# Optimization experiments

Measured on AMD Instinct MI355X. Metric: run time of the kernel, lower is better.

The kernel has to match this reference:

```python
import jax, jax.numpy as jnp
import numpy as np
import math

B, C, H, W = 32, 128, 32, 32
NUM_HEADS = 4
GROUPS = 32
EPS = 1e-5


def setup_inputs() -> dict:
    key = jax.random.key(0)
    ks = jax.random.split(key, 6)
    x = jax.random.normal(ks[0], (B, C, H, W), jnp.float32)
    norm_w = 1.0 + 0.1 * jax.random.normal(ks[1], (C,), jnp.float32)
    norm_b = 0.1 * jax.random.normal(ks[2], (C,), jnp.float32)
    qkv_w = jax.random.normal(ks[3], (3 * C, C), jnp.float32) / math.sqrt(C)
    proj_w = jax.random.normal(ks[4], (C, C), jnp.float32) / math.sqrt(C)
    proj_b = 0.01 * jax.random.normal(ks[5], (C,), jnp.float32)
    return {"x": x, "norm_w": norm_w, "norm_b": norm_b, "qkv_w": qkv_w,
            "proj_w": proj_w, "proj_b": proj_b}


def _group_norm(x, w, b):
    b_, c, h, w_ = x.shape
    xg = x.reshape(b_, GROUPS, c // GROUPS, h, w_)
    mu = xg.mean(axis=(2, 3, 4), keepdims=True)
    var = xg.var(axis=(2, 3, 4), keepdims=True)
    xn = ((xg - mu) * jax.lax.rsqrt(var + EPS)).reshape(b_, c, h, w_)
    return xn * w[None, :, None, None] + b[None, :, None, None]


def reference(x, norm_w, norm_b, qkv_w, proj_w, proj_b):
    b, c, h, w = x.shape
    nh = NUM_HEADS
    dh = c // nh
    hw = h * w
    xn = _group_norm(x, norm_w, norm_b)
    # 1x1 conv (no bias): [B,3C,H,W] flattened to [B,3C,HW]
    qkv = jnp.einsum('oc,bchw->bohw', qkv_w, xn).reshape(b, nh, 3 * dh, hw)
    # torch reshape (B*nh, 3C/nh, HW) + chunk(3, dim=1): per-head interleave
    q, k, v = qkv[:, :, :dh], qkv[:, :, dh:2 * dh], qkv[:, :, 2 * dh:]
    scale = 1.0 / math.sqrt(dh)
    # scale applied to BOTH q and k, as in the source
    attn = jnp.einsum('bhct,bhcs->bhts', q * scale, k * scale)  # [B,nh,HW,HW]
    attn = jax.nn.softmax(attn, axis=-1)
    hout = jnp.einsum('bhts,bhcs->bhct', attn, v).reshape(b, c, h, w)
    hout = jnp.einsum('oc,bchw->bohw', proj_w, hout) + proj_b[None, :, None, None]
    return hout + x
```

## Files before the change

### kernel.cpp

```cpp
#include <hip/hip_runtime.h>
#include <math.h>

#define BB 32
#define CC 128
#define HW 1024
#define NG 32
#define TPG 4096
#define QSZ ((size_t)BB * 4 * HW * 32)

typedef __attribute__((ext_vector_type(8))) short fragAB;
typedef __attribute__((ext_vector_type(4))) float fragC;
typedef __attribute__((ext_vector_type(8))) ushort ushort8v;

__device__ __forceinline__ ushort f2bf(float f) {
  union { float f; uint u; } v; v.f = f;
  uint r = v.u + 0x7FFFu + ((v.u >> 16) & 1u);
  return (ushort)(r >> 16);
}
__device__ __forceinline__ uint pack2(float lo, float hi) {
  return __builtin_amdgcn_perm(__float_as_uint(hi), __float_as_uint(lo), 0x07060302u);
}
__device__ __forceinline__ int vswz(int row, int g) {
  return row * 128 + 16 * (g ^ (row & 7));
}

__global__ __launch_bounds__(256) void gn_stats(const float* __restrict__ x,
    float2* __restrict__ stats, const float* __restrict__ qkvw,
    const float* __restrict__ projw, ushort* __restrict__ wq16,
    ushort* __restrict__ wp16) {
  if (blockIdx.x >= 1024) {
    int idx = (blockIdx.x - 1024) * 256 + threadIdx.x;
    if (idx < 49152) wq16[idx] = f2bf(qkvw[idx]);
    else             wp16[idx - 49152] = f2bf(projw[idx - 49152]);
    return;
  }
  int blk = blockIdx.x;
  int b = blk >> 5, g = blk & 31;
  const float4* xp4 = (const float4*)(x + ((size_t)(b * CC + g * 4)) * HW);
  float s = 0.f, s2 = 0.f;
  #pragma unroll
  for (int i = 0; i < 4; ++i) {
    float4 v = xp4[threadIdx.x + i * 256];
    s  += v.x + v.y + v.z + v.w;
    s2 += v.x * v.x + v.y * v.y + v.z * v.z + v.w * v.w;
  }
  #pragma unroll
  for (int off = 32; off; off >>= 1) {
    s  += __shfl_down(s, off, 64);
    s2 += __shfl_down(s2, off, 64);
  }
  __shared__ float ls[4], ls2[4];
  int lane = threadIdx.x & 63, wid = threadIdx.x >> 6;
  if (lane == 0) { ls[wid] = s; ls2[wid] = s2; }
  __syncthreads();
  if (threadIdx.x == 0) {
    float a  = ls[0] + ls[1] + ls[2] + ls[3];
    float a2 = ls2[0] + ls2[1] + ls2[2] + ls2[3];
    float mu = a * (1.f / TPG);
    float var = a2 * (1.f / TPG) - mu * mu;
    stats[blk] = make_float2(mu, rsqrtf(var + 1e-5f));
  }
}

__global__ __launch_bounds__(256) void mgemm_qkv(
    const ushort* __restrict__ W16, const float* __restrict__ xf,
    const float2* __restrict__ stats, const float* __restrict__ gw,
    const float* __restrict__ gb, ushort* __restrict__ Qb) {
  __shared__ ushort Xs[64 * 128];
  int b = blockIdx.z, t0 = blockIdx.x * 64;
  int tid = threadIdx.x;
  int lane = tid & 63, w = tid >> 6, lc = lane & 15, lg = lane >> 4;
  int wo = w >> 1, wt = w & 1;

  {
    int tq = tid & 15, co = tid >> 4;
    const float* xb = xf + (size_t)b * CC * HW + t0 + tq * 4;
    float wsc[8], bsc[8];
    {
      float2 s0 = stats[b * 32 + co * 2];
      float2 s1 = stats[b * 32 + co * 2 + 1];
      #pragma unroll
      for (int cc = 0; cc < 8; ++cc) {
        float rst = (cc < 4) ? s0.y : s1.y;
        float mu  = (cc < 4) ? s0.x : s1.x;
        float g = gw[co * 8 + cc];
        wsc[cc] = g * rst;
        bsc[cc] = gb[co * 8 + cc] - mu * wsc[cc];
      }
    }
    union { float4 v; float f[4]; } vv[8];
    #pragma unroll
    for (int cc = 0; cc < 8; ++cc)
      vv[cc].v = *(const float4*)&xb[(size_t)(co * 8 + cc) * HW];
    #pragma unroll
    for (int tt = 0; tt < 4; ++tt) {
      int row = tq * 4 + tt;
      ushort8v r;
      #pragma unroll
      for (int cc = 0; cc < 8; ++cc)
        r[cc] = f2bf(vv[cc].f[tt] * wsc[cc] + bsc[cc]);
      int byt = (row * 256 + co * 16) ^ ((row & 7) << 4);
      *(ushort8v*)((char*)Xs + byt) = r;
    }
  }
  __syncthreads();

  auto load_af = [&](fragAB af[2][4], int o0) {
    #pragma unroll
    for (int i = 0; i < 2; ++i)
      #pragma unroll
      for (int kc = 0; kc < 4; ++kc)
        af[i][kc] = *(const fragAB*)&W16[(size_t)(o0 + wo * 32 + i * 16 + lc) * 128 + kc * 32 + lg * 8];
  };
  auto kloop = [&](fragAB af[2][4], fragC acc[2][2]) {
    #pragma unroll
    for (int i = 0; i < 2; ++i)
      #pragma unroll
      for (int j = 0; j < 2; ++j)
        acc[i][j] = (fragC){0.f, 0.f, 0.f, 0.f};
    #pragma unroll
    for (int kc = 0; kc < 4; ++kc) {
      fragAB bf[2];
      #pragma unroll
      for (int j = 0; j < 2; ++j) {
        int row = wt * 32 + j * 16 + lc;
        int byt = (row * 256 + kc * 64 + lg * 16) ^ ((row & 7) << 4);
        bf[j] = *(const fragAB*)((const char*)Xs + byt);
      }
      #pragma unroll
      for (int i = 0; i < 2; ++i)
        #pragma unroll
        for (int j = 0; j < 2; ++j)
          acc[i][j] = __builtin_amdgcn_mfma_f32_16x16x32_bf16(af[i][kc], bf[j], acc[i][j], 0, 0, 0);
    }
  };
  auto epi = [&](fragC acc[2][2], int o0) {
    #pragma unroll
    for (int i = 0; i < 2; ++i) {
      int ob = o0 + wo * 32 + i * 16;
      int blk = ob >> 5;
      int hh = blk / 3, kind = blk % 3;
      size_t bh = (size_t)b * 4 + hh;
      float sc = (kind == 0) ? (0.03125f * 1.44269504f) : 1.f;
      #pragma unroll
      for (int j = 0; j < 2; ++j) {
        if (kind < 2) {
          ushort* dst = (kind == 0) ? Qb : (Qb + QSZ);
          int s16 = (t0 >> 4) + wt * 2 + j;
          int eo = s16 * 512 + (((ob & 16) >> 3) + (lg >> 1)) * 128 + lc * 8 + (lg & 1) * 4;
          ushort4 rv;
          rv.x = f2bf(acc[i][j][0] * sc); rv.y = f2bf(acc[i][j][1] * sc);
          rv.z = f2bf(acc[i][j][2] * sc); rv.w = f2bf(acc[i][j][3] * sc);
          *(ushort4*)&dst[bh * 32768 + eo] = rv;
        } else {
          ushort* Vb = Qb + 2 * QSZ;
          int eo = (t0 >> 6) * 2048 + ((ob & 16) >> 4) * 1024
                 + (wt * 4 + j * 2 + (lc >> 3)) * 128 + (lc & 7);
          #pragma unroll
          for (int r = 0; r < 4; ++r)
            Vb[bh * 32768 + eo + (lg * 4 + r) * 8] = f2bf(acc[i][j][r]);
        }
      }
    }
  };

  fragAB afA[2][4], afB[2][4];
  fragC acc[2][2];
  load_af(afA, 0);
  load_af(afB, 64);
  kloop(afA, acc); epi(acc, 0);   load_af(afA, 128);
  kloop(afB, acc); epi(acc, 64);  load_af(afB, 192);
  kloop(afA, acc); epi(acc, 128); load_af(afA, 256);
  kloop(afB, acc); epi(acc, 192); load_af(afB, 320);
  kloop(afA, acc); epi(acc, 256);
  kloop(afB, acc); epi(acc, 320);
}

__global__ __launch_bounds__(512) void attn9(
    const ushort* __restrict__ Qb, const ushort* __restrict__ Kb,
    const ushort* __restrict__ Vb, const ushort* __restrict__ wp16,
    const float* __restrict__ bias, const float* __restrict__ resid,
    float* __restrict__ out) {
  __shared__ char arena[33792];

  int tid = threadIdx.x;
  int w = tid >> 6, lane = tid & 63, lc = lane & 15, lg = lane >> 4;
  int lb = blockIdx.x;
  int gp = (lb & 7) * 64 + (lb >> 3);
  int b = gp >> 4, qp = gp & 15;
  int h = w >> 1, qs = w & 1;
  int bh = b * 4 + h;
  int t0 = qp * 64;
  int qt = qp * 2 + qs;

  const ushort* Qg = Qb + (size_t)bh * 32768 + (size_t)qt * 1024 + lane * 8;
  const ushort* Kg = Kb + (size_t)bh * 32768 + lane * 8;
  const ushort* Vg = Vb + (size_t)bh * 32768 + lane * 8;

  fragAB q0 = *(const fragAB*)&Qg[0];
  fragAB q1 = *(const fragAB*)&Qg[512];

  fragC a00 = {0.f,0.f,0.f,0.f}, a01 = {0.f,0.f,0.f,0.f};
  fragC a10 = {0.f,0.f,0.f,0.f}, a11 = {0.f,0.f,0.f,0.f};
  float l0 = 0.f, l1 = 0.f;
  char* PsB = arena + w * 2048;

  for (int i = 0; i < 16; ++i) {
    const ushort* Kt = Kg + i * 2048;
    const ushort* Vt = Vg + i * 2048;
    fragAB kf[4], vf[4];
    #pragma unroll
    for (int j = 0; j < 4; ++j) kf[j] = *(const fragAB*)&Kt[j * 512];
    #pragma unroll
    for (int u = 0; u < 4; ++u) vf[u] = *(const fragAB*)&Vt[u * 512];

    #pragma unroll
    for (int ts = 0; ts < 2; ++ts) {
      fragAB qf = ts ? q1 : q0;
      fragC S[4];
      #pragma unroll
      for (int j = 0; j < 4; ++j) {
        fragC z = {0.f,0.f,0.f,0.f};
        S[j] = __builtin_amdgcn_mfma_f32_16x16x32_bf16(kf[j], qf, z, 0, 0, 0);
      }
      float rs = 0.f;
      #pragma unroll
      for (int j = 0; j < 4; ++j) {
        float p0 = __builtin_amdgcn_exp2f(S[j][0]), p1 = __builtin_amdgcn_exp2f(S[j][1]);
        float p2 = __builtin_amdgcn_exp2f(S[j][2]), p3 = __builtin_amdgcn_exp2f(S[j][3]);
        rs += (p0 + p1) + (p2 + p3);
        uint2 wv2;
        wv2.x = pack2(p0, p1);
        wv2.y = pack2(p2, p3);
        int g = j * 2 + (lg >> 1);
        *(uint2*)(PsB + lc * 128 + 16 * (g ^ (lc & 7)) + (lg & 1) * 8) = wv2;
      }
      if (ts) l1 += rs; else l0 += rs;
      fragC* aA = ts ? &a01 : &a00;
      fragC* aB = ts ? &a11 : &a10;
      fragAB bp0 = *(const fragAB*)(PsB + vswz(lc, lg));
      fragAB bp1 = *(const fragAB*)(PsB + vswz(lc, 4 + lg));
      *aA = __builtin_amdgcn_mfma_f32_16x16x32_bf16(vf[0], bp0, *aA, 0, 0, 0);
      *aA = __builtin_amdgcn_mfma_f32_16x16x32_bf16(vf[1], bp1, *aA, 0, 0, 0);
      *aB = __builtin_amdgcn_mfma_f32_16x16x32_bf16(vf[2], bp0, *aB, 0, 0, 0);
      *aB = __builtin_amdgcn_mfma_f32_16x16x32_bf16(vf[3], bp1, *aB, 0, 0, 0);
    }
  }

  l0 += __shfl_xor(l0, 16); l0 += __shfl_xor(l0, 32);
  l1 += __shfl_xor(l1, 16); l1 += __shfl_xor(l1, 32);
  float il0 = 1.f / l0, il1 = 1.f / l1;

  ushort* Olds = (ushort*)(arena + 16384);
  {
    int rb = qs * 32, cb = h * 32;
    uint2 u;
    u.x = pack2(a00[0] * il0, a00[1] * il0); u.y = pack2(a00[2] * il0, a00[3] * il0);
    *(uint2*)&Olds[(rb + lc) * 136 + cb + lg * 4] = u;
    u.x = pack2(a10[0] * il0, a10[1] * il0); u.y = pack2(a10[2] * il0, a10[3] * il0);
    *(uint2*)&Olds[(rb + lc) * 136 + cb + 16 + lg * 4] = u;
    u.x = pack2(a01[0] * il1, a01[1] * il1); u.y = pack2(a01[2] * il1, a01[3] * il1);
    *(uint2*)&Olds[(rb + lc + 16) * 136 + cb + lg * 4] = u;
    u.x = pack2(a11[0] * il1, a11[1] * il1); u.y = pack2(a11[2] * il1, a11[3] * il1);
    *(uint2*)&Olds[(rb + lc + 16) * 136 + cb + 16 + lg * 4] = u;
  }
  __syncthreads();

  fragC pacc[4] = {{0.f,0.f,0.f,0.f}, {0.f,0.f,0.f,0.f},
                   {0.f,0.f,0.f,0.f}, {0.f,0.f,0.f,0.f}};
  #pragma unroll
  for (int kc = 0; kc < 4; ++kc) {
    fragAB af = *(const fragAB*)&wp16[(size_t)(16 * w + lc) * 128 + kc * 32 + lg * 8];
    #pragma unroll
    for (int j = 0; j < 4; ++j) {
      fragAB bf = *(const fragAB*)&Olds[(j * 16 + lc) * 136 + kc * 32 + lg * 8];
      pacc[j] = __builtin_amdgcn_mfma_f32_16x16x32_bf16(af, bf, pacc[j], 0, 0, 0);
    }
  }
  #pragma unroll
  for (int j = 0; j < 4; ++j) {
    int t = t0 + j * 16 + lc;
    #pragma unroll
    for (int r = 0; r < 4; ++r) {
      int o = 16 * w + lg * 4 + r;
      size_t idx = ((size_t)b * CC + o) * HW + t;
      out[idx] = pacc[j][r] + bias[o] + resid[idx];
    }
  }
}

extern "C" void kernel_launch(void* const* d_in, const int* in_sizes, int n_in,
                              void* d_out, int out_size, void* d_ws, size_t ws_size,
                              hipStream_t stream) {
  (void)in_sizes; (void)n_in; (void)out_size; (void)ws_size;
  const float* x     = (const float*)d_in[0];
  const float* gw    = (const float*)d_in[1];
  const float* gb    = (const float*)d_in[2];
  const float* qkvw  = (const float*)d_in[3];
  const float* projw = (const float*)d_in[4];
  const float* projb = (const float*)d_in[5];
  float* out = (float*)d_out;

  char* wsb = (char*)d_ws;
  ushort* Qb   = (ushort*)(wsb + ((size_t)8 << 20));
  ushort* Kb   = Qb + QSZ;
  ushort* Vb   = Qb + 2 * QSZ;
  ushort* wq16 = (ushort*)(wsb + ((size_t)32 << 20));
  ushort* wp16 = (ushort*)(wsb + ((size_t)32 << 20) + (128 << 10));
  float2* stats = (float2*)(wsb + ((size_t)32 << 20) + (256 << 10));

  gn_stats<<<dim3(BB * NG + 256), 256, 0, stream>>>(x, stats, qkvw, projw, wq16, wp16);
  mgemm_qkv<<<dim3(16, 1, BB), 256, 0, stream>>>(wq16, x, stats, gw, gb, Qb);
  attn9<<<dim3(512), 512, 0, stream>>>(Qb, Kb, Vb, wp16, projb, x, out);
}
```

Measured before the change: 58.49 us.

## Enlarge attention blocks to 128 query positions with 16 waves and 2x2 projection tiles

The fused attention+projection kernel now uses 1024-thread blocks covering 128 query positions per batch, with 16 waves (4 heads x 4 query slices). There are half as many blocks. The output projection is retiled so each wave computes a 32x32 tile and reuses A and B fragments. The O staging buffer now reuses the start of the LDS arena, which needs an extra barrier. The aim is better reuse of projection weights and fewer blocks, at the cost of a larger block that may reduce occupancy or load balance across 256 CUs.

```diff
diff --git a/kernel.cpp b/kernel.cpp
--- a/kernel.cpp
+++ b/kernel.cpp
@@ -176,22 +176,21 @@
   kloop(afB, acc); epi(acc, 320);
 }
 
-__global__ __launch_bounds__(512) void attn9(
+__global__ __launch_bounds__(1024) void attn11(
     const ushort* __restrict__ Qb, const ushort* __restrict__ Kb,
     const ushort* __restrict__ Vb, const ushort* __restrict__ wp16,
     const float* __restrict__ bias, const float* __restrict__ resid,
     float* __restrict__ out) {
-  __shared__ char arena[33792];
+  __shared__ char arena[34816];
 
   int tid = threadIdx.x;
   int w = tid >> 6, lane = tid & 63, lc = lane & 15, lg = lane >> 4;
   int lb = blockIdx.x;
-  int gp = (lb & 7) * 64 + (lb >> 3);
-  int b = gp >> 4, qp = gp & 15;
-  int h = w >> 1, qs = w & 1;
+  int gp = (lb & 7) * 32 + (lb >> 3);
+  int b = gp >> 3, qp = gp & 7;
+  int h = w & 3, qs = w >> 2;
   int bh = b * 4 + h;
-  int t0 = qp * 64;
-  int qt = qp * 2 + qs;
+  int qt = qp * 4 + qs;
 
   const ushort* Qg = Qb + (size_t)bh * 32768 + (size_t)qt * 1024 + lane * 8;
   const ushort* Kg = Kb + (size_t)bh * 32768 + lane * 8;
@@ -251,7 +250,9 @@
   l1 += __shfl_xor(l1, 16); l1 += __shfl_xor(l1, 32);
   float il0 = 1.f / l0, il1 = 1.f / l1;
 
-  ushort* Olds = (ushort*)(arena + 16384);
+  __syncthreads();
+
+  ushort* Olds = (ushort*)arena;
   {
     int rb = qs * 32, cb = h * 32;
     uint2 u;
@@ -266,27 +267,36 @@
   }
   __syncthreads();
 
-  fragC pacc[4] = {{0.f,0.f,0.f,0.f}, {0.f,0.f,0.f,0.f},
-                   {0.f,0.f,0.f,0.f}, {0.f,0.f,0.f,0.f}};
+  int oi = w & 3, tj = w >> 2;
+  fragC pacc[2][2] = {{{0.f,0.f,0.f,0.f}, {0.f,0.f,0.f,0.f}},
+                      {{0.f,0.f,0.f,0.f}, {0.f,0.f,0.f,0.f}}};
   #pragma unroll
   for (int kc = 0; kc < 4; ++kc) {
-    fragAB af = *(const fragAB*)&wp16[(size_t)(16 * w + lc) * 128 + kc * 32 + lg * 8];
-    #pragma unroll
-    for (int j = 0; j < 4; ++j) {
-      fragAB bf = *(const fragAB*)&Olds[(j * 16 + lc) * 136 + kc * 32 + lg * 8];
-      pacc[j] = __builtin_amdgcn_mfma_f32_16x16x32_bf16(af, bf, pacc[j], 0, 0, 0);
-    }
+    fragAB af[2], bf[2];
+    #pragma unroll
+    for (int i = 0; i < 2; ++i)
+      af[i] = *(const fragAB*)&wp16[(size_t)(oi * 32 + i * 16 + lc) * 128 + kc * 32 + lg * 8];
+    #pragma unroll
+    for (int j = 0; j < 2; ++j)
+      bf[j] = *(const fragAB*)&Olds[(tj * 32 + j * 16 + lc) * 136 + kc * 32 + lg * 8];
+    #pragma unroll
+    for (int i = 0; i < 2; ++i)
+      #pragma unroll
+      for (int j = 0; j < 2; ++j)
+        pacc[i][j] = __builtin_amdgcn_mfma_f32_16x16x32_bf16(af[i], bf[j], pacc[i][j], 0, 0, 0);
   }
   #pragma unroll
-  for (int j = 0; j < 4; ++j) {
-    int t = t0 + j * 16 + lc;
-    #pragma unroll
-    for (int r = 0; r < 4; ++r) {
-      int o = 16 * w + lg * 4 + r;
-      size_t idx = ((size_t)b * CC + o) * HW + t;
-      out[idx] = pacc[j][r] + bias[o] + resid[idx];
-    }
-  }
+  for (int i = 0; i < 2; ++i)
+    #pragma unroll
+    for (int j = 0; j < 2; ++j) {
+      int t = qp * 128 + tj * 32 + j * 16 + lc;
+      #pragma unroll
+      for (int r = 0; r < 4; ++r) {
+        int o = oi * 32 + i * 16 + lg * 4 + r;
+        size_t idx = ((size_t)b * CC + o) * HW + t;
+        out[idx] = pacc[i][j][r] + bias[o] + resid[idx];
+      }
+    }
 }
 
 extern "C" void kernel_launch(void* const* d_in, const int* in_sizes, int n_in,
@@ -311,5 +321,5 @@
 
   gn_stats<<<dim3(BB * NG + 256), 256, 0, stream>>>(x, stats, qkvw, projw, wq16, wp16);
   mgemm_qkv<<<dim3(16, 1, BB), 256, 0, stream>>>(wq16, x, stats, gw, gb, Qb);
-  attn9<<<dim3(512), 512, 0, stream>>>(Qb, Kb, Vb, wp16, projb, x, out);
-}
+  attn11<<<dim3(256), 1024, 0, stream>>>(Qb, Kb, Vb, wp16, projb, x, out);
+}
```

New measurement: 60.88 us. 4.1% more time.

## Switch attention to 32x32x16 MFMA with permlane-swap P transpose, no LDS

Applied to the files above, without the earlier changes.

Rewrites the attention inner loop to use 32x32x16 bf16 MFMA for both QK^T and PV. The softmax probabilities are converted into the B operand in registers using v_permlane32_swap instead of a round trip through LDS, which removes LDS writes and reads from each tile. The QKV GEMM epilogue is changed to write Q/K/V in a new layout that matches the 32x32 fragment ordering, and the LDS arena is shrunk. The larger 16-float accumulator fragments raise register pressure, and permlane32_swap is specific to newer CDNA parts.

```diff
diff --git a/kernel.cpp b/kernel.cpp
--- a/kernel.cpp
+++ b/kernel.cpp
@@ -10,6 +10,7 @@
 
 typedef __attribute__((ext_vector_type(8))) short fragAB;
 typedef __attribute__((ext_vector_type(4))) float fragC;
+typedef __attribute__((ext_vector_type(16))) float fragC16;
 typedef __attribute__((ext_vector_type(8))) ushort ushort8v;
 
 __device__ __forceinline__ ushort f2bf(float f) {
@@ -19,9 +20,6 @@
 }
 __device__ __forceinline__ uint pack2(float lo, float hi) {
   return __builtin_amdgcn_perm(__float_as_uint(hi), __float_as_uint(lo), 0x07060302u);
-}
-__device__ __forceinline__ int vswz(int row, int g) {
-  return row * 128 + 16 * (g ^ (row & 7));
 }
 
 __global__ __launch_bounds__(256) void gn_stats(const float* __restrict__ x,
@@ -142,23 +140,27 @@
       int hh = blk / 3, kind = blk % 3;
       size_t bh = (size_t)b * 4 + hh;
       float sc = (kind == 0) ? (0.03125f * 1.44269504f) : 1.f;
+      int cb = ob & 16;
       #pragma unroll
       for (int j = 0; j < 2; ++j) {
+        int t = t0 + wt * 32 + j * 16 + lc;
         if (kind < 2) {
           ushort* dst = (kind == 0) ? Qb : (Qb + QSZ);
-          int s16 = (t0 >> 4) + wt * 2 + j;
-          int eo = s16 * 512 + (((ob & 16) >> 3) + (lg >> 1)) * 128 + lc * 8 + (lg & 1) * 4;
+          int c4 = cb + lg * 4;
+          int eo = (t >> 5) * 1024 + (c4 >> 4) * 512 + (((c4 >> 3) & 1)) * 256
+                 + (t & 31) * 8 + (c4 & 7);
           ushort4 rv;
           rv.x = f2bf(acc[i][j][0] * sc); rv.y = f2bf(acc[i][j][1] * sc);
           rv.z = f2bf(acc[i][j][2] * sc); rv.w = f2bf(acc[i][j][3] * sc);
           *(ushort4*)&dst[bh * 32768 + eo] = rv;
         } else {
           ushort* Vb = Qb + 2 * QSZ;
-          int eo = (t0 >> 6) * 2048 + ((ob & 16) >> 4) * 1024
-                 + (wt * 4 + j * 2 + (lc >> 3)) * 128 + (lc & 7);
+          int sb = (t >> 4) * 512 + ((t >> 3) & 1) * 256 + (t & 7);
           #pragma unroll
-          for (int r = 0; r < 4; ++r)
-            Vb[bh * 32768 + eo + (lg * 4 + r) * 8] = f2bf(acc[i][j][r]);
+          for (int r = 0; r < 4; ++r) {
+            int c = cb + lg * 4 + r;
+            Vb[bh * 32768 + sb + c * 8] = f2bf(acc[i][j][r]);
+          }
         }
       }
     }
@@ -176,15 +178,16 @@
   kloop(afB, acc); epi(acc, 320);
 }
 
-__global__ __launch_bounds__(512) void attn9(
+__global__ __launch_bounds__(512) void attn12(
     const ushort* __restrict__ Qb, const ushort* __restrict__ Kb,
     const ushort* __restrict__ Vb, const ushort* __restrict__ wp16,
     const float* __restrict__ bias, const float* __restrict__ resid,
     float* __restrict__ out) {
-  __shared__ char arena[33792];
+  __shared__ char arena[17408];
 
   int tid = threadIdx.x;
   int w = tid >> 6, lane = tid & 63, lc = lane & 15, lg = lane >> 4;
+  int t = lane & 31, hi = lane >> 5;
   int lb = blockIdx.x;
   int gp = (lb & 7) * 64 + (lb >> 3);
   int b = gp >> 4, qp = gp & 15;
@@ -197,72 +200,71 @@
   const ushort* Kg = Kb + (size_t)bh * 32768 + lane * 8;
   const ushort* Vg = Vb + (size_t)bh * 32768 + lane * 8;
 
-  fragAB q0 = *(const fragAB*)&Qg[0];
-  fragAB q1 = *(const fragAB*)&Qg[512];
-
-  fragC a00 = {0.f,0.f,0.f,0.f}, a01 = {0.f,0.f,0.f,0.f};
-  fragC a10 = {0.f,0.f,0.f,0.f}, a11 = {0.f,0.f,0.f,0.f};
-  float l0 = 0.f, l1 = 0.f;
-  char* PsB = arena + w * 2048;
+  fragAB qf0 = *(const fragAB*)&Qg[0];
+  fragAB qf1 = *(const fragAB*)&Qg[512];
+
+  fragC16 acc = {0.f,0.f,0.f,0.f,0.f,0.f,0.f,0.f,0.f,0.f,0.f,0.f,0.f,0.f,0.f,0.f};
+  float l = 0.f;
+
+  auto stile = [&](fragAB ka, fragAB kb, fragAB va, fragAB vb) {
+    fragC16 S = {0.f,0.f,0.f,0.f,0.f,0.f,0.f,0.f,0.f,0.f,0.f,0.f,0.f,0.f,0.f,0.f};
+    S = __builtin_amdgcn_mfma_f32_32x32x16_bf16(ka, qf0, S, 0, 0, 0);
+    S = __builtin_amdgcn_mfma_f32_32x32x16_bf16(kb, qf1, S, 0, 0, 0);
+    float p[16];
+    float rs = 0.f;
+    #pragma unroll
+    for (int r = 0; r < 16; ++r) { p[r] = __builtin_amdgcn_exp2f(S[r]); rs += p[r]; }
+    l += rs;
+    uint U[8];
+    #pragma unroll
+    for (int k = 0; k < 8; ++k) U[k] = pack2(p[2 * k], p[2 * k + 1]);
+    uint A[8], Bv[8];
+    #pragma unroll
+    for (int m = 0; m < 8; ++m) {
+      uint a = U[m], bb = U[m];
+      asm volatile("v_permlane32_swap_b32 %0, %1" : "+v"(a), "+v"(bb));
+      A[m] = a; Bv[m] = bb;
+    }
+    union { uint u[4]; fragAB f; } bf;
+    bf.u[0] = hi ? A[2] : A[0];
+    bf.u[1] = hi ? A[3] : A[1];
+    bf.u[2] = hi ? Bv[2] : Bv[0];
+    bf.u[3] = hi ? Bv[3] : Bv[1];
+    acc = __builtin_amdgcn_mfma_f32_32x32x16_bf16(va, bf.f, acc, 0, 0, 0);
+    bf.u[0] = hi ? A[6] : A[4];
+    bf.u[1] = hi ? A[7] : A[5];
+    bf.u[2] = hi ? Bv[6] : Bv[4];
+    bf.u[3] = hi ? Bv[7] : Bv[5];
+    acc = __builtin_amdgcn_mfma_f32_32x32x16_bf16(vb, bf.f, acc, 0, 0, 0);
+  };
 
   for (int i = 0; i < 16; ++i) {
     const ushort* Kt = Kg + i * 2048;
     const ushort* Vt = Vg + i * 2048;
-    fragAB kf[4], vf[4];
-    #pragma unroll
-    for (int j = 0; j < 4; ++j) kf[j] = *(const fragAB*)&Kt[j * 512];
-    #pragma unroll
-    for (int u = 0; u < 4; ++u) vf[u] = *(const fragAB*)&Vt[u * 512];
-
-    #pragma unroll
-    for (int ts = 0; ts < 2; ++ts) {
-      fragAB qf = ts ? q1 : q0;
-      fragC S[4];
-      #pragma unroll
-      for (int j = 0; j < 4; ++j) {
-        fragC z = {0.f,0.f,0.f,0.f};
-        S[j] = __builtin_amdgcn_mfma_f32_16x16x32_bf16(kf[j], qf, z, 0, 0, 0);
-      }
-      float rs = 0.f;
-      #pragma unroll
-      for (int j = 0; j < 4; ++j) {
-        float p0 = __builtin_amdgcn_exp2f(S[j][0]), p1 = __builtin_amdgcn_exp2f(S[j][1]);
-        float p2 = __builtin_amdgcn_exp2f(S[j][2]), p3 = __builtin_amdgcn_exp2f(S[j][3]);
-        rs += (p0 + p1) + (p2 + p3);
-        uint2 wv2;
-        wv2.x = pack2(p0, p1);
-        wv2.y = pack2(p2, p3);
-        int g = j * 2 + (lg >> 1);
-        *(uint2*)(PsB + lc * 128 + 16 * (g ^ (lc & 7)) + (lg & 1) * 8) = wv2;
-      }
-      if (ts) l1 += rs; else l0 += rs;
-      fragC* aA = ts ? &a01 : &a00;
-      fragC* aB = ts ? &a11 : &a10;
-      fragAB bp0 = *(const fragAB*)(PsB + vswz(lc, lg));
-      fragAB bp1 = *(const fragAB*)(PsB + vswz(lc, 4 + lg));
-      *aA = __builtin_amdgcn_mfma_f32_16x16x32_bf16(vf[0], bp0, *aA, 0, 0, 0);
-      *aA = __builtin_amdgcn_mfma_f32_16x16x32_bf16(vf[1], bp1, *aA, 0, 0, 0);
-      *aB = __builtin_amdgcn_mfma_f32_16x16x32_bf16(vf[2], bp0, *aB, 0, 0, 0);
-      *aB = __builtin_amdgcn_mfma_f32_16x16x32_bf16(vf[3], bp1, *aB, 0, 0, 0);
-    }
-  }
-
-  l0 += __shfl_xor(l0, 16); l0 += __shfl_xor(l0, 32);
-  l1 += __shfl_xor(l1, 16); l1 += __shfl_xor(l1, 32);
-  float il0 = 1.f / l0, il1 = 1.f / l1;
-
-  ushort* Olds = (ushort*)(arena + 16384);
+    fragAB kf00 = *(const fragAB*)&Kt[0];
+    fragAB kf01 = *(const fragAB*)&Kt[512];
+    fragAB kf10 = *(const fragAB*)&Kt[1024];
+    fragAB kf11 = *(const fragAB*)&Kt[1536];
+    fragAB vf0 = *(const fragAB*)&Vt[0];
+    fragAB vf1 = *(const fragAB*)&Vt[512];
+    fragAB vf2 = *(const fragAB*)&Vt[1024];
+    fragAB vf3 = *(const fragAB*)&Vt[1536];
+    stile(kf00, kf01, vf0, vf1);
+    stile(kf10, kf11, vf2, vf3);
+  }
+
+  l += __shfl_xor(l, 32);
+  float il = 1.f / l;
+
+  ushort* Olds = (ushort*)arena;
   {
-    int rb = qs * 32, cb = h * 32;
-    uint2 u;
-    u.x = pack2(a00[0] * il0, a00[1] * il0); u.y = pack2(a00[2] * il0, a00[3] * il0);
-    *(uint2*)&Olds[(rb + lc) * 136 + cb + lg * 4] = u;
-    u.x = pack2(a10[0] * il0, a10[1] * il0); u.y = pack2(a10[2] * il0, a10[3] * il0);
-    *(uint2*)&Olds[(rb + lc) * 136 + cb + 16 + lg * 4] = u;
-    u.x = pack2(a01[0] * il1, a01[1] * il1); u.y = pack2(a01[2] * il1, a01[3] * il1);
-    *(uint2*)&Olds[(rb + lc + 16) * 136 + cb + lg * 4] = u;
-    u.x = pack2(a11[0] * il1, a11[1] * il1); u.y = pack2(a11[2] * il1, a11[3] * il1);
-    *(uint2*)&Olds[(rb + lc + 16) * 136 + cb + 16 + lg * 4] = u;
+    int rb = qs * 32, cbh = h * 32;
+    #pragma unroll
+    for (int k = 0; k < 8; ++k) {
+      uint u = pack2(acc[2 * k] * il, acc[2 * k + 1] * il);
+      int c = 8 * (k >> 1) + 4 * hi + 2 * (k & 1);
+      *(uint*)&Olds[(rb + t) * 136 + cbh + c] = u;
+    }
   }
   __syncthreads();
 
@@ -279,11 +281,11 @@
   }
   #pragma unroll
   for (int j = 0; j < 4; ++j) {
-    int t = t0 + j * 16 + lc;
+    int tt = t0 + j * 16 + lc;
     #pragma unroll
     for (int r = 0; r < 4; ++r) {
       int o = 16 * w + lg * 4 + r;
-      size_t idx = ((size_t)b * CC + o) * HW + t;
+      size_t idx = ((size_t)b * CC + o) * HW + tt;
       out[idx] = pacc[j][r] + bias[o] + resid[idx];
     }
   }
@@ -311,5 +313,5 @@
 
   gn_stats<<<dim3(BB * NG + 256), 256, 0, stream>>>(x, stats, qkvw, projw, wq16, wp16);
   mgemm_qkv<<<dim3(16, 1, BB), 256, 0, stream>>>(wq16, x, stats, gw, gb, Qb);
-  attn9<<<dim3(512), 512, 0, stream>>>(Qb, Kb, Vb, wp16, projb, x, out);
-}
+  attn12<<<dim3(512), 512, 0, stream>>>(Qb, Kb, Vb, wp16, projb, x, out);
+}
```

Measured after the change: 61.59 us. 5.3% more time.
